# Optimization experiments

Measured on AMD Instinct MI355X. Metric: run time of the kernel, lower is better.

## Reference

```python
import jax, jax.numpy as jnp
import numpy as np

EMBED_DIM = 1024
HEAD_SIZE = 64
B, T = 4, 4096


def setup_inputs() -> dict:
    key = jax.random.key(0)
    kx, kq, kk, kv = jax.random.split(key, 4)
    x = jax.random.normal(kx, (B, T, EMBED_DIM), dtype=jnp.float32)
    sw = 1.0 / np.sqrt(EMBED_DIM)  # kaiming-ish init scale for linear weights
    Wq = jax.random.normal(kq, (EMBED_DIM, HEAD_SIZE), dtype=jnp.float32) * sw
    Wk = jax.random.normal(kk, (EMBED_DIM, HEAD_SIZE), dtype=jnp.float32) * sw
    Wv = jax.random.normal(kv, (EMBED_DIM, HEAD_SIZE), dtype=jnp.float32) * sw
    return {"x": x, "Wq": Wq, "Wk": Wk, "Wv": Wv}


def reference(x, Wq, Wk, Wv):
    Bn, Tn, C = x.shape
    q = jnp.einsum('btc,ch->bth', x, Wq)
    k = jnp.einsum('btc,ch->bth', x, Wk)
    v = jnp.einsum('btc,ch->bth', x, Wv)
    # NOTE: original scales by sqrt(C) = sqrt(embed_dim), not sqrt(head_size)
    scale = 1.0 / jnp.sqrt(jnp.asarray(C, dtype=x.dtype))
    wei = jnp.einsum('bth,bsh->bts', q, k) * scale  # [B, T, T]
    causal = jnp.tril(jnp.ones((Tn, Tn), dtype=bool))
    wei = jnp.where(causal, wei, -jnp.inf)
    wei = jax.nn.softmax(wei, axis=-1)
    # dropout p=0.0 (eval mode): identity
    return jnp.einsum('bts,bsh->bth', wei, v)
```

## Files before the change

kernel.cpp:

```cpp
#include <hip/hip_runtime.h>
#include <cstdint>


typedef __bf16 bf16;
typedef __bf16 bf16x4 __attribute__((ext_vector_type(4)));
typedef __bf16 bf16x8 __attribute__((ext_vector_type(8)));
typedef float  f32x4  __attribute__((ext_vector_type(4)));

#define MFMA16(a, b, c) __builtin_amdgcn_mfma_f32_16x16x32_bf16((a), (b), (c), 0, 0, 0)

#if __has_builtin(__builtin_amdgcn_exp2f)
#define EXP2(x) __builtin_amdgcn_exp2f(x)
#else
#define EXP2(x) exp2f(x)
#endif

#define B_SZ 4
#define T_SZ 4096
#define C_SZ 1024
#define H_SZ 64
#define M_SZ (B_SZ * T_SZ)
#define QSCALE (1.4426950408889634f / 32.0f)
#define P_O 8192
#define P_L 128

__device__ __forceinline__ void dma16(const void* g, void* l) {
    __builtin_amdgcn_global_load_lds(
        (const __attribute__((address_space(1))) uint32_t*)(uintptr_t)g,
        (__attribute__((address_space(3))) uint32_t*)(uint32_t)(uintptr_t)l,
        16, 0, 0);
}

#define WAIT_BARRIER(N) do {                                       \
    asm volatile("s_waitcnt vmcnt(" #N ")" ::: "memory");          \
    __builtin_amdgcn_s_barrier();                                  \
    __builtin_amdgcn_sched_barrier(0);                             \
} while (0)

#define BOT_BARRIER() do {                                         \
    __builtin_amdgcn_sched_barrier(0);                             \
    __builtin_amdgcn_s_barrier();                                  \
    __builtin_amdgcn_sched_barrier(0);                             \
} while (0)

__global__ __launch_bounds__(256) void wt_prep(
    const float* __restrict__ Wq, const float* __restrict__ Wk,
    const float* __restrict__ Wv, bf16* __restrict__ wt2)
{
    const int n4 = blockIdx.x, t = threadIdx.x;
    const int nbase = n4 * 4;
    const float* W = (nbase < 64) ? Wq : (nbase < 128 ? Wk : Wv);
    const float sc = (nbase < 64) ? QSCALE : 1.0f;
    const int ncol = nbase & 63;
    #pragma unroll
    for (int i = 0; i < 4; ++i) {
        const int k = i * 256 + t;
        const float4 v = *(const float4*)(W + (size_t)k * H_SZ + ncol);
        const float vals[4] = {v.x, v.y, v.z, v.w};
        const size_t base = (size_t)(k >> 6) * 12288 + (size_t)((k >> 5) & 1) * 6144
                          + (size_t)((k >> 3) & 3) * 1536 + (k & 7);
        #pragma unroll
        for (int m = 0; m < 4; ++m)
            wt2[base + (size_t)(nbase + m) * 8] = (bf16)(vals[m] * sc);
    }
}

__global__ __launch_bounds__(512) void qkv_proj(
    const float* __restrict__ x, const bf16* __restrict__ wt2,
    bf16* __restrict__ qw, bf16* __restrict__ kw2, bf16* __restrict__ vtw2)
{
    const int m0 = blockIdx.x * 64;
    const int tid = threadIdx.x;
    const int wave = tid >> 6, lane = tid & 63;
    const int quad = lane >> 4, l15 = lane & 15;
    const int rh = wave >> 2;
    const int cg = wave & 3;
    const int phase = blockIdx.x & 15;

    __shared__ __align__(16) float xs[2][64 * 64];
    __shared__ __align__(16) bf16  ws[2][2 * 4 * 192 * 8];

    f32x4 acc[2][3] = {};

    const int r0 = tid >> 4;
    const int csrc = (tid & 15) ^ (r0 & 7);
    const char* xg0 = (const char*)x + (size_t)(m0 + r0) * 4096 + (size_t)csrc * 16;
    const char* xg1 = xg0 + (size_t)32 * 4096;
    const char* wg = (const char*)wt2 + (size_t)tid * 16;

    auto stage = [&](int s, int buf) {
        const size_t se = (size_t)((s + phase) & 15);
        char* xl = (char*)(&xs[buf][0]) + (size_t)tid * 16;
        char* wl = (char*)(&ws[buf][0]) + (size_t)tid * 16;
        dma16(xg0 + se * 256, xl);
        dma16(xg1 + se * 256, xl + 8192);
        #pragma unroll
        for (int i = 0; i < 3; ++i)
            dma16(wg + se * 24576 + (size_t)i * 8192, wl + (size_t)i * 8192);
    };

    stage(0, 0);

    for (int s = 0; s < 16; ++s) {
        if (s < 15) {
            stage(s + 1, (s + 1) & 1);
            WAIT_BARRIER(5);
        } else {
            WAIT_BARRIER(0);
        }
        const float* xb = &xs[s & 1][0];
        const bf16*  wb = &ws[s & 1][0];

        #pragma unroll
        for (int ss = 0; ss < 2; ++ss) {
            bf16x8 a[2];
            const int cbase = ss * 8 + quad * 2;
            #pragma unroll
            for (int mg = 0; mg < 2; ++mg) {
                const int row = rh * 32 + mg * 16 + l15;
                const int rx = row & 7;
                const float* xrow = xb + row * 64;
                const f32x4 lo = *(const f32x4*)(xrow + ((cbase ^ rx) << 2));
                const f32x4 hi = *(const f32x4*)(xrow + (((cbase + 1) ^ rx) << 2));
                a[mg][0] = (bf16)lo[0]; a[mg][1] = (bf16)lo[1];
                a[mg][2] = (bf16)lo[2]; a[mg][3] = (bf16)lo[3];
                a[mg][4] = (bf16)hi[0]; a[mg][5] = (bf16)hi[1];
                a[mg][6] = (bf16)hi[2]; a[mg][7] = (bf16)hi[3];
            }
            #pragma unroll
            for (int i = 0; i < 3; ++i) {
                const int nt = cg * 3 + i;
                const bf16x8 wf = *(const bf16x8*)(wb + ss * 6144 + quad * 1536
                                                   + (nt * 16 + l15) * 8);
                #pragma unroll
                for (int mg = 0; mg < 2; ++mg)
                    acc[mg][i] = MFMA16(a[mg], wf, acc[mg][i]);
            }
        }

        BOT_BARRIER();
    }

    #pragma unroll
    for (int mg = 0; mg < 2; ++mg)
        #pragma unroll
        for (int i = 0; i < 3; ++i) {
            const int n = (cg * 3 + i) * 16 + l15;
            const int which = n >> 6, col = n & 63;
            #pragma unroll
            for (int r = 0; r < 4; ++r) {
                const int t = m0 + rh * 32 + mg * 16 + quad * 4 + r;
                const bf16 v = (bf16)acc[mg][i][r];
                if (which == 0) {
                    qw[(size_t)t * H_SZ + col] = v;
                } else if (which == 1) {
                    kw2[(size_t)(t >> 6) * 4096
                        + (size_t)(((col >> 5) << 2) + ((col >> 3) & 3)) * 512
                        + (size_t)(t & 63) * 8 + (col & 7)] = v;
                } else {
                    const int t6 = t & 63;
                    const int p = ((t6 >> 2) & 3) * 8 + (t6 & 3) * 2
                                + ((t6 >> 4) & 1) + (t6 >> 5) * 32;
                    vtw2[(size_t)(t >> 6) * 4096
                         + (size_t)(p >> 3) * 512 + (size_t)col * 8 + (p & 7)] = v;
                }
            }
        }
}

__global__ __launch_bounds__(256) void flash_attn(
    const bf16* __restrict__ qw, const bf16* __restrict__ kw2,
    const bf16* __restrict__ vtw2, bf16* __restrict__ pbuf_o,
    float* __restrict__ pbuf_l)
{
    const int bx = blockIdx.x;
    const int item = (bx & 1) ? (511 - (bx >> 1)) : (bx >> 1);
    const int qt2 = 31 - (item >> 4);
    const int b   = (item >> 2) & 3;
    const int h   = item & 3;
    const int i0  = qt2 * 128;
    const int nkv = qt2 * 2 + 2;

    const int tid = threadIdx.x;
    const int wave = tid >> 6, lane = tid & 63;
    const int quad = lane >> 4, l15 = lane & 15;

    __shared__ __align__(16) bf16 kvs[2][8192];

    bf16x8 aq[2][2];
    #pragma unroll
    for (int mg2 = 0; mg2 < 2; ++mg2) {
        const bf16* qp = qw + ((size_t)b * T_SZ + i0 + wave * 32 + mg2 * 16 + l15) * H_SZ
                       + quad * 8;
        aq[mg2][0] = *(const bf16x8*)qp;
        aq[mg2][1] = *(const bf16x8*)(qp + 32);
    }
    const bf16 onev = (bf16)1.0f;
    const bf16x8 vone = {onev, onev, onev, onev, onev, onev, onev, onev};

    const char* kgb = (const char*)kw2 + (size_t)b * 524288;
    const char* vgb = (const char*)vtw2 + (size_t)b * 524288;

    f32x4 o[2][4] = {};
    f32x4 osum[2] = {};

    auto stage = [&](int jt, int buf) {
        const char* ks = kgb + (size_t)jt * 8192;
        const char* vs = vgb + (size_t)jt * 8192;
        char* dst = (char*)(&kvs[buf][0]) + (size_t)tid * 16;
        dma16(ks + (size_t)tid * 16, dst);
        dma16(ks + 4096 + (size_t)tid * 16, dst + 4096);
        dma16(vs + (size_t)tid * 16, dst + 8192);
        dma16(vs + 4096 + (size_t)tid * 16, dst + 12288);
    };

    if (h < nkv) stage(h, 0);

    int c = 0;
    for (int jt = h; jt < nkv; jt += 4, c ^= 1) {
        if (jt + 4 < nkv) {
            stage(jt + 4, c ^ 1);
            WAIT_BARRIER(4);
        } else {
            WAIT_BARRIER(0);
        }
        const bf16* kb = &kvs[c][0];
        const bf16* vb = &kvs[c][0] + 4096;

        f32x4 s4t[4][2] = {};
        __builtin_amdgcn_s_setprio(1);
        #pragma unroll
        for (int ct = 0; ct < 4; ++ct) {
            const bf16x8 k0 = *(const bf16x8*)(kb + (0 * 4 + quad) * 512 + (ct * 16 + l15) * 8);
            const bf16x8 k1 = *(const bf16x8*)(kb + (1 * 4 + quad) * 512 + (ct * 16 + l15) * 8);
            #pragma unroll
            for (int mg2 = 0; mg2 < 2; ++mg2) {
                s4t[ct][mg2] = MFMA16(k0, aq[mg2][0], s4t[ct][mg2]);
                s4t[ct][mg2] = MFMA16(k1, aq[mg2][1], s4t[ct][mg2]);
            }
        }
        __builtin_amdgcn_s_setprio(0);

        if (jt >= 2 * qt2) {
            #pragma unroll
            for (int mg2 = 0; mg2 < 2; ++mg2) {
                const int gq = i0 + wave * 32 + mg2 * 16 + l15;
                #pragma unroll
                for (int ct = 0; ct < 4; ++ct) {
                    const int gkv0 = jt * 64 + ct * 16 + quad * 4;
                    #pragma unroll
                    for (int rr = 0; rr < 4; ++rr)
                        if (gkv0 + rr > gq) s4t[ct][mg2][rr] = -3.0e38f;
                }
            }
        }

        bf16x8 pa[2][2];
        #pragma unroll
        for (int mg2 = 0; mg2 < 2; ++mg2)
            #pragma unroll
            for (int j = 0; j < 8; ++j) {
                pa[mg2][0][j] = (bf16)EXP2(s4t[j & 1][mg2][j >> 1]);
                pa[mg2][1][j] = (bf16)EXP2(s4t[2 + (j & 1)][mg2][j >> 1]);
            }

        __builtin_amdgcn_s_setprio(1);
        #pragma unroll
        for (int ht = 0; ht < 4; ++ht) {
            const bf16x8 v0 = *(const bf16x8*)(vb + (0 * 4 + quad) * 512 + (ht * 16 + l15) * 8);
            const bf16x8 v1 = *(const bf16x8*)(vb + (1 * 4 + quad) * 512 + (ht * 16 + l15) * 8);
            #pragma unroll
            for (int mg2 = 0; mg2 < 2; ++mg2) {
                o[mg2][ht] = MFMA16(pa[mg2][0], v0, o[mg2][ht]);
                o[mg2][ht] = MFMA16(pa[mg2][1], v1, o[mg2][ht]);
            }
        }
        #pragma unroll
        for (int mg2 = 0; mg2 < 2; ++mg2) {
            osum[mg2] = MFMA16(pa[mg2][0], vone, osum[mg2]);
            osum[mg2] = MFMA16(pa[mg2][1], vone, osum[mg2]);
        }
        __builtin_amdgcn_s_setprio(0);

        BOT_BARRIER();
    }

    bf16* pb_o = pbuf_o + (size_t)(((b * 32 + qt2) * 4) + h) * P_O;
    float* pb_l = pbuf_l + (size_t)(((b * 32 + qt2) * 4) + h) * P_L;
    #pragma unroll
    for (int mg2 = 0; mg2 < 2; ++mg2) {
        const int L0 = wave * 32 + mg2 * 16 + quad * 4;
        #pragma unroll
        for (int ht = 0; ht < 4; ++ht)
            #pragma unroll
            for (int rr = 0; rr < 4; ++rr)
                pb_o[(L0 + rr) * 64 + ht * 16 + l15] = (bf16)o[mg2][ht][rr];
        if (l15 == 0) {
            #pragma unroll
            for (int rr = 0; rr < 4; ++rr)
                pb_l[L0 + rr] = osum[mg2][rr];
        }
    }
}

__global__ __launch_bounds__(256) void combine(
    const bf16* __restrict__ pbuf_o, const float* __restrict__ pbuf_l,
    float* __restrict__ out)
{
    const int bq2 = blockIdx.x >> 1, tid = threadIdx.x;
    const int row = ((blockIdx.x & 1) << 6) + (tid >> 2);
    const int c0 = (tid & 3) * 16;

    float a[16] = {};
    float l = 0.f;
    #pragma unroll
    for (int h = 0; h < 4; ++h) {
        const bf16* ph = pbuf_o + (size_t)(bq2 * 4 + h) * P_O + row * 64 + c0;
        const bf16x8 v0 = *(const bf16x8*)ph;
        const bf16x8 v1 = *(const bf16x8*)(ph + 8);
        #pragma unroll
        for (int j = 0; j < 8; ++j) {
            a[j]     += (float)v0[j];
            a[8 + j] += (float)v1[j];
        }
        l += pbuf_l[(size_t)(bq2 * 4 + h) * P_L + row];
    }
    const float inv = 1.0f / l;
    float* op = out + ((size_t)bq2 * 128 + row) * 64 + c0;
    #pragma unroll
    for (int g = 0; g < 4; ++g) {
        f32x4 v = {a[g * 4], a[g * 4 + 1], a[g * 4 + 2], a[g * 4 + 3]};
        *(f32x4*)(op + g * 4) = v * inv;
    }
}

extern "C" void kernel_launch(void* const* d_in, const int* in_sizes, int n_in,
                              void* d_out, int out_size, void* d_ws, size_t ws_size,
                              hipStream_t stream) {
    const float* x  = (const float*)d_in[0];
    const float* Wq = (const float*)d_in[1];
    const float* Wk = (const float*)d_in[2];
    const float* Wv = (const float*)d_in[3];

    bf16* qw   = (bf16*)d_ws;
    bf16* kw2  = qw + (size_t)M_SZ * H_SZ;
    bf16* vtw2 = kw2 + (size_t)M_SZ * H_SZ;
    bf16* wt2  = vtw2 + (size_t)M_SZ * H_SZ;
    bf16* pbuf_o = wt2 + 3 * 64 * 1024;
    float* pbuf_l = (float*)(pbuf_o + (size_t)512 * P_O);
    float* out = (float*)d_out;

    wt_prep<<<48, 256, 0, stream>>>(Wq, Wk, Wv, wt2);
    qkv_proj<<<M_SZ / 64, 512, 0, stream>>>(x, wt2, qw, kw2, vtw2);
    flash_attn<<<512, 256, 0, stream>>>(qw, kw2, vtw2, pbuf_o, pbuf_l);
    combine<<<256, 256, 0, stream>>>(pbuf_o, pbuf_l, out);
}
```

Baseline: 132.8 us.

## Convert x tile to bf16 in registers before LDS store in QKV projection

In qkv_proj, the x tile was previously DMA'd as fp32 into LDS and converted to bf16 at every fragment read. It is now loaded into registers with global loads, converted to bf16 once, and written to a swizzled bf16 LDS buffer after the current step's MFMAs. This halves LDS footprint and read traffic for x and drops the per-read conversions, at the cost of register-staged loads. Barriers now wait for all outstanding loads (vmcnt(0)) plus LDS ops, which may reduce overlap between the global fetch and compute.

```diff
diff --git a/kernel.cpp b/kernel.cpp
--- a/kernel.cpp
+++ b/kernel.cpp
@@ -31,16 +31,17 @@
         16, 0, 0);
 }
 
-#define WAIT_BARRIER(N) do {                                       \
-    asm volatile("s_waitcnt vmcnt(" #N ")" ::: "memory");          \
-    __builtin_amdgcn_s_barrier();                                  \
-    __builtin_amdgcn_sched_barrier(0);                             \
+#define WAIT_BARRIER(N) do {                                           \
+    asm volatile("s_waitcnt vmcnt(" #N ") lgkmcnt(0)" ::: "memory");   \
+    __builtin_amdgcn_s_barrier();                                      \
+    __builtin_amdgcn_sched_barrier(0);                                 \
 } while (0)
 
-#define BOT_BARRIER() do {                                         \
-    __builtin_amdgcn_sched_barrier(0);                             \
-    __builtin_amdgcn_s_barrier();                                  \
-    __builtin_amdgcn_sched_barrier(0);                             \
+#define BOT_BARRIER() do {                                             \
+    __builtin_amdgcn_sched_barrier(0);                                 \
+    asm volatile("s_waitcnt lgkmcnt(0)" ::: "memory");                 \
+    __builtin_amdgcn_s_barrier();                                      \
+    __builtin_amdgcn_sched_barrier(0);                                 \
 } while (0)
 
 __global__ __launch_bounds__(256) void wt_prep(
@@ -77,55 +78,64 @@
     const int cg = wave & 3;
     const int phase = blockIdx.x & 15;
 
-    __shared__ __align__(16) float xs[2][64 * 64];
-    __shared__ __align__(16) bf16  ws[2][2 * 4 * 192 * 8];
+    __shared__ __align__(16) bf16 xs[2][64 * 64];
+    __shared__ __align__(16) bf16 ws[2][2 * 4 * 192 * 8];
 
     f32x4 acc[2][3] = {};
 
     const int r0 = tid >> 4;
-    const int csrc = (tid & 15) ^ (r0 & 7);
-    const char* xg0 = (const char*)x + (size_t)(m0 + r0) * 4096 + (size_t)csrc * 16;
+    const int hh = tid & 15;
+    const char* xg0 = (const char*)x + (size_t)(m0 + r0) * 4096 + (size_t)hh * 16;
     const char* xg1 = xg0 + (size_t)32 * 4096;
     const char* wg = (const char*)wt2 + (size_t)tid * 16;
-
-    auto stage = [&](int s, int buf) {
+    const int xoff0 = r0 * 128 + ((((hh >> 1)) ^ (r0 & 7)) << 4) + ((hh & 1) << 3);
+    const int xoff1 = xoff0 + 32 * 128;
+
+    auto stage_w = [&](int s, int buf) {
         const size_t se = (size_t)((s + phase) & 15);
-        char* xl = (char*)(&xs[buf][0]) + (size_t)tid * 16;
         char* wl = (char*)(&ws[buf][0]) + (size_t)tid * 16;
-        dma16(xg0 + se * 256, xl);
-        dma16(xg1 + se * 256, xl + 8192);
         #pragma unroll
         for (int i = 0; i < 3; ++i)
             dma16(wg + se * 24576 + (size_t)i * 8192, wl + (size_t)i * 8192);
     };
-
-    stage(0, 0);
+    auto write_x = [&](const float4& L0, const float4& L1, int buf) {
+        bf16x4 c0, c1;
+        c0[0] = (bf16)L0.x; c0[1] = (bf16)L0.y; c0[2] = (bf16)L0.z; c0[3] = (bf16)L0.w;
+        c1[0] = (bf16)L1.x; c1[1] = (bf16)L1.y; c1[2] = (bf16)L1.z; c1[3] = (bf16)L1.w;
+        *(bf16x4*)((char*)(&xs[buf][0]) + xoff0) = c0;
+        *(bf16x4*)((char*)(&xs[buf][0]) + xoff1) = c1;
+    };
+
+    {
+        const size_t se = (size_t)(phase & 15);
+        const float4 P0 = *(const float4*)(xg0 + se * 256);
+        const float4 P1 = *(const float4*)(xg1 + se * 256);
+        stage_w(0, 0);
+        write_x(P0, P1, 0);
+    }
 
     for (int s = 0; s < 16; ++s) {
+        WAIT_BARRIER(0);
+
+        float4 L0, L1;
         if (s < 15) {
-            stage(s + 1, (s + 1) & 1);
-            WAIT_BARRIER(5);
-        } else {
-            WAIT_BARRIER(0);
-        }
-        const float* xb = &xs[s & 1][0];
-        const bf16*  wb = &ws[s & 1][0];
+            const size_t se = (size_t)((s + 1 + phase) & 15);
+            L0 = *(const float4*)(xg0 + se * 256);
+            L1 = *(const float4*)(xg1 + se * 256);
+            stage_w(s + 1, (s + 1) & 1);
+        }
+
+        const bf16* xb = &xs[s & 1][0];
+        const bf16* wb = &ws[s & 1][0];
 
         #pragma unroll
         for (int ss = 0; ss < 2; ++ss) {
             bf16x8 a[2];
-            const int cbase = ss * 8 + quad * 2;
             #pragma unroll
             for (int mg = 0; mg < 2; ++mg) {
                 const int row = rh * 32 + mg * 16 + l15;
-                const int rx = row & 7;
-                const float* xrow = xb + row * 64;
-                const f32x4 lo = *(const f32x4*)(xrow + ((cbase ^ rx) << 2));
-                const f32x4 hi = *(const f32x4*)(xrow + (((cbase + 1) ^ rx) << 2));
-                a[mg][0] = (bf16)lo[0]; a[mg][1] = (bf16)lo[1];
-                a[mg][2] = (bf16)lo[2]; a[mg][3] = (bf16)lo[3];
-                a[mg][4] = (bf16)hi[0]; a[mg][5] = (bf16)hi[1];
-                a[mg][6] = (bf16)hi[2]; a[mg][7] = (bf16)hi[3];
+                a[mg] = *(const bf16x8*)((const char*)xb + row * 128
+                         + (((ss * 4 + quad) ^ (row & 7)) << 4));
             }
             #pragma unroll
             for (int i = 0; i < 3; ++i) {
@@ -137,6 +147,8 @@
                     acc[mg][i] = MFMA16(a[mg], wf, acc[mg][i]);
             }
         }
+
+        if (s < 15) write_x(L0, L1, (s + 1) & 1);
 
         BOT_BARRIER();
     }
```

Result: slower. 138.9 us (+4.6%).
